# Optimization experiments

Measured on AMD Instinct MI355X. Metric: run time of the kernel, lower is better.

The kernel has to match this reference:

```python
import jax, jax.numpy as jnp
import numpy as np

N_NODES = 100000
N_EDGES = 800000
IN_FEAT = 128


def setup_inputs() -> dict:
    key = jax.random.key(0)
    k_feat, k_src, k_dst, k_w1, k_b1, k_w2 = jax.random.split(key, 6)
    feature = jax.random.normal(k_feat, (N_NODES, IN_FEAT), dtype=jnp.float32)
    src = jax.random.randint(k_src, (N_EDGES,), 0, N_NODES, dtype=jnp.int64)
    dst = jax.random.randint(k_dst, (N_EDGES,), 0, N_NODES, dtype=jnp.int64)
    # nn.Linear params: y = x @ W.T + b; Kaiming-uniform-ish init scale
    lim1 = 1.0 / np.sqrt(2 * IN_FEAT)
    W1 = jax.random.uniform(k_w1, (IN_FEAT, 2 * IN_FEAT), jnp.float32, -lim1, lim1)
    b1 = jax.random.uniform(k_b1, (IN_FEAT,), jnp.float32, -lim1, lim1)
    lim2 = 1.0 / np.sqrt(IN_FEAT)
    W2 = jax.random.uniform(k_w2, (1, IN_FEAT), jnp.float32, -lim2, lim2)
    b2 = jnp.zeros((1,), jnp.float32)
    return {"feature": feature, "src": src, "dst": dst,
            "W1": W1, "b1": b1, "W2": W2, "b2": b2}


def reference(feature, src, dst, W1, b1, W2, b2):
    # gather src/dst node feats and concat -> [E, 2*in_feat]
    h = jnp.concatenate([feature[src], feature[dst]], axis=1)
    # 2-layer MLP per edge: Linear -> ReLU -> Linear
    hid = jax.nn.relu(h @ W1.T + b1)            # [E, in_feat]
    score = hid @ W2.T + b2                      # [E, 1]
    return score
```

## Files before the change

### kernel.cpp

```cpp
#include <hip/hip_runtime.h>
#include <stdint.h>

typedef short short8 __attribute__((ext_vector_type(8)));
typedef float floatx4 __attribute__((ext_vector_type(4)));

#define NN 100000
#define NE 800000
#define KF 128
#define PC 256
#define BM 64
#define LDK 136

__device__ __forceinline__ unsigned short f2bf(float x) {
  union { float f; unsigned u; } c; c.f = x;
  unsigned u = c.u + 0x7FFFu + ((c.u >> 16) & 1u);
  return (unsigned short)(u >> 16);
}
__device__ __forceinline__ float bfl(unsigned u) {
  union { unsigned u; float f; } c; c.u = u << 16; return c.f;
}
__device__ __forceinline__ float bfh(unsigned u) {
  union { unsigned u; float f; } c; c.u = u & 0xFFFF0000u; return c.f;
}

extern "C" __global__ void __launch_bounds__(256)
wcat_prep_kernel(const float* __restrict__ W1, unsigned short* __restrict__ Wcatb)
{
  const int idx = blockIdx.x * 256 + threadIdx.x;
  const int j  = idx >> 4;
  const int k8 = (idx & 15) << 3;

  const int h  = j >> 7;
  const int jl = j & 127;
  const float* sp = W1 + (size_t)jl * 256 + h * 128 + k8;
  const float4 f0 = ((const float4*)sp)[0];
  const float4 f1 = ((const float4*)sp)[1];

  short8 v;
  v[0] = (short)f2bf(f0.x); v[1] = (short)f2bf(f0.y);
  v[2] = (short)f2bf(f0.z); v[3] = (short)f2bf(f0.w);
  v[4] = (short)f2bf(f1.x); v[5] = (short)f2bf(f1.y);
  v[6] = (short)f2bf(f1.z); v[7] = (short)f2bf(f1.w);

  const unsigned lin = (unsigned)jl * 256u + (unsigned)k8 * 2u;
  const unsigned swz = lin ^ ((unsigned)(jl & 7) << 4);
  *(short8*)((char*)Wcatb + h * 32768 + swz) = v;
}

extern "C" __global__ void __launch_bounds__(256)
node_proj_kernel(const float* __restrict__ feature,
                 const unsigned short* __restrict__ Wcatb,
                 const float* __restrict__ b1,
                 unsigned short* __restrict__ P)
{
  __shared__ unsigned short Wl[128 * 128];
  __shared__ unsigned short Al[BM * LDK];
  __shared__ float b1l[128];

  const int t = threadIdx.x;
  const int nodeBase = blockIdx.x * BM;

  #pragma unroll
  for (int it = 0; it < 8; ++it) {
    int c = t + it * 256;
    __builtin_amdgcn_global_load_lds(
        (const __attribute__((address_space(1))) void*)((const char*)Wcatb + c * 16),
        (__attribute__((address_space(3))) void*)((char*)Wl + c * 16),
        16, 0, 0);
  }

  #pragma unroll
  for (int it = 0; it < 4; ++it) {
    int c  = t + it * 256;
    int nl = c >> 4;
    int kc = (c & 15) << 3;
    int node = nodeBase + nl;
    float4 f0 = make_float4(0.f, 0.f, 0.f, 0.f);
    float4 f1 = make_float4(0.f, 0.f, 0.f, 0.f);
    if (node < NN) {
      const float* fp = feature + (size_t)node * KF + kc;
      f0 = ((const float4*)fp)[0];
      f1 = ((const float4*)fp)[1];
    }
    short8 v;
    v[0] = (short)f2bf(f0.x); v[1] = (short)f2bf(f0.y);
    v[2] = (short)f2bf(f0.z); v[3] = (short)f2bf(f0.w);
    v[4] = (short)f2bf(f1.x); v[5] = (short)f2bf(f1.y);
    v[6] = (short)f2bf(f1.z); v[7] = (short)f2bf(f1.w);
    *(short8*)&Al[nl * LDK + kc] = v;
  }
  if (t < 128) b1l[t] = b1[t];

  const int wave = t >> 6;
  const int lane = t & 63;
  const int m16  = lane & 15;
  const int quad = lane >> 4;

  short8 a0, a1, a2, a3;
  bool aLoaded = false;

  for (int half = 0; half < 2; ++half) {
    __syncthreads();

    if (!aLoaded) {
      const unsigned short* arow = &Al[(wave * 16 + m16) * LDK + quad * 8];
      a0 = *(const short8*)(arow + 0);
      a1 = *(const short8*)(arow + 32);
      a2 = *(const short8*)(arow + 64);
      a3 = *(const short8*)(arow + 96);
      aLoaded = true;
    }

    #pragma unroll
    for (int nt = 0; nt < 8; ++nt) {
      floatx4 acc = {0.f, 0.f, 0.f, 0.f};
      const int j = nt * 16 + m16;
      const unsigned base = (unsigned)j * 256u + (unsigned)quad * 16u;
      const unsigned msk  = (unsigned)(j & 7) << 4;
      const char* WlB = (const char*)Wl;
      acc = __builtin_amdgcn_mfma_f32_16x16x32_bf16(a0, *(const short8*)(WlB + ((base +   0u) ^ msk)), acc, 0, 0, 0);
      acc = __builtin_amdgcn_mfma_f32_16x16x32_bf16(a1, *(const short8*)(WlB + ((base +  64u) ^ msk)), acc, 0, 0, 0);
      acc = __builtin_amdgcn_mfma_f32_16x16x32_bf16(a2, *(const short8*)(WlB + ((base + 128u) ^ msk)), acc, 0, 0, 0);
      acc = __builtin_amdgcn_mfma_f32_16x16x32_bf16(a3, *(const short8*)(WlB + ((base + 192u) ^ msk)), acc, 0, 0, 0);

      const int n = half * 128 + j;
      const float bias = (half == 0) ? b1l[j] : 0.f;
      #pragma unroll
      for (int r = 0; r < 4; ++r) {
        int node = nodeBase + wave * 16 + quad * 4 + r;
        if (node < NN) P[(size_t)node * PC + n] = f2bf(acc[r] + bias);
      }
    }

    if (half == 0) {
      __syncthreads();
      #pragma unroll
      for (int it = 0; it < 8; ++it) {
        int c = t + it * 256;
        __builtin_amdgcn_global_load_lds(
            (const __attribute__((address_space(1))) void*)((const char*)Wcatb + 32768 + c * 16),
            (__attribute__((address_space(3))) void*)((char*)Wl + c * 16),
            16, 0, 0);
      }
    }
  }
}

__device__ __forceinline__ float dot8(const uint4 u1, const uint4 u2,
                                      const float4 wA, const float4 wB)
{
  float acc = 0.f, x;
  x = fmaxf(bfl(u1.x) + bfl(u2.x), 0.f); acc += x * wA.x;
  x = fmaxf(bfh(u1.x) + bfh(u2.x), 0.f); acc += x * wA.y;
  x = fmaxf(bfl(u1.y) + bfl(u2.y), 0.f); acc += x * wA.z;
  x = fmaxf(bfh(u1.y) + bfh(u2.y), 0.f); acc += x * wA.w;
  x = fmaxf(bfl(u1.z) + bfl(u2.z), 0.f); acc += x * wB.x;
  x = fmaxf(bfh(u1.z) + bfh(u2.z), 0.f); acc += x * wB.y;
  x = fmaxf(bfl(u1.w) + bfl(u2.w), 0.f); acc += x * wB.z;
  x = fmaxf(bfh(u1.w) + bfh(u2.w), 0.f); acc += x * wB.w;
  return acc;
}

extern "C" __global__ void __launch_bounds__(256)
edge_score_kernel(const unsigned short* __restrict__ P,
                  const int* __restrict__ src,
                  const int* __restrict__ dst,
                  const float* __restrict__ W2,
                  const float* __restrict__ b2,
                  float* __restrict__ out)
{
  const int t    = threadIdx.x;
  const int lane = t & 15;
  const int g    = t >> 4;
  const int e0   = blockIdx.x * 64 + g * 4;
  if (e0 >= NE) return;

  const int4 sv = *(const int4*)(src + e0);
  const int4 dv = *(const int4*)(dst + e0);

  const unsigned short* Ps = P + lane * 8;
  const unsigned short* Pd = P + 128 + lane * 8;

  const uint4 A0 = *(const uint4*)(Ps + (size_t)sv.x * PC);
  const uint4 B0 = *(const uint4*)(Pd + (size_t)dv.x * PC);
  const uint4 A1 = *(const uint4*)(Ps + (size_t)sv.y * PC);
  const uint4 B1 = *(const uint4*)(Pd + (size_t)dv.y * PC);
  const uint4 A2 = *(const uint4*)(Ps + (size_t)sv.z * PC);
  const uint4 B2 = *(const uint4*)(Pd + (size_t)dv.z * PC);
  const uint4 A3 = *(const uint4*)(Ps + (size_t)sv.w * PC);
  const uint4 B3 = *(const uint4*)(Pd + (size_t)dv.w * PC);

  const float4 wA = *(const float4*)(W2 + lane * 8);
  const float4 wB = *(const float4*)(W2 + lane * 8 + 4);

  float r0 = dot8(A0, B0, wA, wB);
  float r1 = dot8(A1, B1, wA, wB);
  float r2 = dot8(A2, B2, wA, wB);
  float r3 = dot8(A3, B3, wA, wB);

  r0 += __shfl_xor(r0, 8); r1 += __shfl_xor(r1, 8);
  r2 += __shfl_xor(r2, 8); r3 += __shfl_xor(r3, 8);
  r0 += __shfl_xor(r0, 4); r1 += __shfl_xor(r1, 4);
  r2 += __shfl_xor(r2, 4); r3 += __shfl_xor(r3, 4);
  r0 += __shfl_xor(r0, 2); r1 += __shfl_xor(r1, 2);
  r2 += __shfl_xor(r2, 2); r3 += __shfl_xor(r3, 2);
  r0 += __shfl_xor(r0, 1); r1 += __shfl_xor(r1, 1);
  r2 += __shfl_xor(r2, 1); r3 += __shfl_xor(r3, 1);

  if (lane == 0) {
    const float bb = b2[0];
    float4 o;
    o.x = r0 + bb; o.y = r1 + bb; o.z = r2 + bb; o.w = r3 + bb;
    *(float4*)(out + e0) = o;
  }
}

extern "C" void kernel_launch(void* const* d_in, const int* in_sizes, int n_in,
                              void* d_out, int out_size, void* d_ws, size_t ws_size,
                              hipStream_t stream)
{
  const float* feature = (const float*)d_in[0];
  const int*   src     = (const int*)d_in[1];
  const int*   dst     = (const int*)d_in[2];
  const float* W1      = (const float*)d_in[3];
  const float* b1      = (const float*)d_in[4];
  const float* W2      = (const float*)d_in[5];
  const float* b2      = (const float*)d_in[6];
  float* out = (float*)d_out;
  unsigned short* P = (unsigned short*)d_ws;
  unsigned short* Wcatb = (unsigned short*)d_out;

  dim3 gridW(16);
  wcat_prep_kernel<<<gridW, 256, 0, stream>>>(W1, Wcatb);

  dim3 grid1((NN + BM - 1) / BM);
  node_proj_kernel<<<grid1, 256, 0, stream>>>(feature, Wcatb, b1, P);

  dim3 grid2((NE + 63) / 64);
  edge_score_kernel<<<grid2, 256, 0, stream>>>(P, src, dst, W2, b2, out);
}
```

Measured before the change: 170.4 us.

## Quantize per-node projections to int8 with per-row scales for edge gather

The per-node projected hidden halves are now stored as int8 with a per-node, per-half absmax scale instead of bf16. This halves the bytes each edge gathers from the random-access projection table, and it also halves the projection write traffic. In exchange there is an extra scale gather per endpoint, a cross-lane max reduction in the projection kernel, and byte-wise stores with extra dequantization arithmetic. Accuracy loss from int8 rounding of pre-ReLU activations may exceed the tolerance.

Measured after the change: 144.5 us. -15.2%, faster.

```diff
diff --git a/kernel.cpp b/kernel.cpp
--- a/kernel.cpp
+++ b/kernel.cpp
@@ -16,11 +16,8 @@
   unsigned u = c.u + 0x7FFFu + ((c.u >> 16) & 1u);
   return (unsigned short)(u >> 16);
 }
-__device__ __forceinline__ float bfl(unsigned u) {
-  union { unsigned u; float f; } c; c.u = u << 16; return c.f;
-}
-__device__ __forceinline__ float bfh(unsigned u) {
-  union { unsigned u; float f; } c; c.u = u & 0xFFFF0000u; return c.f;
+__device__ __forceinline__ float sb8(unsigned u, int k) {
+  return (float)(signed char)((u >> (8 * k)) & 0xffu);
 }
 
 extern "C" __global__ void __launch_bounds__(256)
@@ -51,7 +48,8 @@
 node_proj_kernel(const float* __restrict__ feature,
                  const unsigned short* __restrict__ Wcatb,
                  const float* __restrict__ b1,
-                 unsigned short* __restrict__ P)
+                 signed char* __restrict__ P,
+                 float* __restrict__ Sc)
 {
   __shared__ unsigned short Wl[128 * 128];
   __shared__ unsigned short Al[BM * LDK];
@@ -111,6 +109,8 @@
       aLoaded = true;
     }
 
+    floatx4 arr[8];
+
     #pragma unroll
     for (int nt = 0; nt < 8; ++nt) {
       floatx4 acc = {0.f, 0.f, 0.f, 0.f};
@@ -122,14 +122,48 @@
       acc = __builtin_amdgcn_mfma_f32_16x16x32_bf16(a1, *(const short8*)(WlB + ((base +  64u) ^ msk)), acc, 0, 0, 0);
       acc = __builtin_amdgcn_mfma_f32_16x16x32_bf16(a2, *(const short8*)(WlB + ((base + 128u) ^ msk)), acc, 0, 0, 0);
       acc = __builtin_amdgcn_mfma_f32_16x16x32_bf16(a3, *(const short8*)(WlB + ((base + 192u) ^ msk)), acc, 0, 0, 0);
-
-      const int n = half * 128 + j;
-      const float bias = (half == 0) ? b1l[j] : 0.f;
-      #pragma unroll
-      for (int r = 0; r < 4; ++r) {
-        int node = nodeBase + wave * 16 + quad * 4 + r;
-        if (node < NN) P[(size_t)node * PC + n] = f2bf(acc[r] + bias);
+      if (half == 0) {
+        const float bias = b1l[j];
+        acc[0] += bias; acc[1] += bias; acc[2] += bias; acc[3] += bias;
       }
+      arr[nt] = acc;
+    }
+
+    float mx0 = 0.f, mx1 = 0.f, mx2 = 0.f, mx3 = 0.f;
+    #pragma unroll
+    for (int nt = 0; nt < 8; ++nt) {
+      mx0 = fmaxf(mx0, fabsf(arr[nt][0]));
+      mx1 = fmaxf(mx1, fabsf(arr[nt][1]));
+      mx2 = fmaxf(mx2, fabsf(arr[nt][2]));
+      mx3 = fmaxf(mx3, fabsf(arr[nt][3]));
+    }
+    #pragma unroll
+    for (int d_ = 1; d_ <= 8; d_ <<= 1) {
+      mx0 = fmaxf(mx0, __shfl_xor(mx0, d_));
+      mx1 = fmaxf(mx1, __shfl_xor(mx1, d_));
+      mx2 = fmaxf(mx2, __shfl_xor(mx2, d_));
+      mx3 = fmaxf(mx3, __shfl_xor(mx3, d_));
+    }
+    const float inv0 = 127.f / fmaxf(mx0, 1e-30f);
+    const float inv1 = 127.f / fmaxf(mx1, 1e-30f);
+    const float inv2 = 127.f / fmaxf(mx2, 1e-30f);
+    const float inv3 = 127.f / fmaxf(mx3, 1e-30f);
+
+    const int n0 = nodeBase + wave * 16 + quad * 4;
+    if (m16 == 0) {
+      if (n0 + 0 < NN) Sc[(size_t)(n0 + 0) * 2 + half] = mx0 * (1.f / 127.f);
+      if (n0 + 1 < NN) Sc[(size_t)(n0 + 1) * 2 + half] = mx1 * (1.f / 127.f);
+      if (n0 + 2 < NN) Sc[(size_t)(n0 + 2) * 2 + half] = mx2 * (1.f / 127.f);
+      if (n0 + 3 < NN) Sc[(size_t)(n0 + 3) * 2 + half] = mx3 * (1.f / 127.f);
+    }
+
+    #pragma unroll
+    for (int nt = 0; nt < 8; ++nt) {
+      const int off = half * 128 + nt * 16 + m16;
+      if (n0 + 0 < NN) P[(size_t)(n0 + 0) * PC + off] = (signed char)(int)rintf(arr[nt][0] * inv0);
+      if (n0 + 1 < NN) P[(size_t)(n0 + 1) * PC + off] = (signed char)(int)rintf(arr[nt][1] * inv1);
+      if (n0 + 2 < NN) P[(size_t)(n0 + 2) * PC + off] = (signed char)(int)rintf(arr[nt][2] * inv2);
+      if (n0 + 3 < NN) P[(size_t)(n0 + 3) * PC + off] = (signed char)(int)rintf(arr[nt][3] * inv3);
     }
 
     if (half == 0) {
@@ -146,23 +180,25 @@
   }
 }
 
-__device__ __forceinline__ float dot8(const uint4 u1, const uint4 u2,
-                                      const float4 wA, const float4 wB)
+__device__ __forceinline__ float dot8i8(const uint2 a, const uint2 b,
+                                        const float sa, const float sb,
+                                        const float* __restrict__ w)
 {
   float acc = 0.f, x;
-  x = fmaxf(bfl(u1.x) + bfl(u2.x), 0.f); acc += x * wA.x;
-  x = fmaxf(bfh(u1.x) + bfh(u2.x), 0.f); acc += x * wA.y;
-  x = fmaxf(bfl(u1.y) + bfl(u2.y), 0.f); acc += x * wA.z;
-  x = fmaxf(bfh(u1.y) + bfh(u2.y), 0.f); acc += x * wA.w;
-  x = fmaxf(bfl(u1.z) + bfl(u2.z), 0.f); acc += x * wB.x;
-  x = fmaxf(bfh(u1.z) + bfh(u2.z), 0.f); acc += x * wB.y;
-  x = fmaxf(bfl(u1.w) + bfl(u2.w), 0.f); acc += x * wB.z;
-  x = fmaxf(bfh(u1.w) + bfh(u2.w), 0.f); acc += x * wB.w;
+  x = fmaxf(fmaf(sb8(a.x, 0), sa, sb8(b.x, 0) * sb), 0.f); acc = fmaf(x, w[0], acc);
+  x = fmaxf(fmaf(sb8(a.x, 1), sa, sb8(b.x, 1) * sb), 0.f); acc = fmaf(x, w[1], acc);
+  x = fmaxf(fmaf(sb8(a.x, 2), sa, sb8(b.x, 2) * sb), 0.f); acc = fmaf(x, w[2], acc);
+  x = fmaxf(fmaf(sb8(a.x, 3), sa, sb8(b.x, 3) * sb), 0.f); acc = fmaf(x, w[3], acc);
+  x = fmaxf(fmaf(sb8(a.y, 0), sa, sb8(b.y, 0) * sb), 0.f); acc = fmaf(x, w[4], acc);
+  x = fmaxf(fmaf(sb8(a.y, 1), sa, sb8(b.y, 1) * sb), 0.f); acc = fmaf(x, w[5], acc);
+  x = fmaxf(fmaf(sb8(a.y, 2), sa, sb8(b.y, 2) * sb), 0.f); acc = fmaf(x, w[6], acc);
+  x = fmaxf(fmaf(sb8(a.y, 3), sa, sb8(b.y, 3) * sb), 0.f); acc = fmaf(x, w[7], acc);
   return acc;
 }
 
 extern "C" __global__ void __launch_bounds__(256)
-edge_score_kernel(const unsigned short* __restrict__ P,
+edge_score_kernel(const signed char* __restrict__ P,
+                  const float* __restrict__ Sc,
                   const int* __restrict__ src,
                   const int* __restrict__ dst,
                   const float* __restrict__ W2,
@@ -178,25 +214,39 @@
   const int4 sv = *(const int4*)(src + e0);
   const int4 dv = *(const int4*)(dst + e0);
 
-  const unsigned short* Ps = P + lane * 8;
-  const unsigned short* Pd = P + 128 + lane * 8;
-
-  const uint4 A0 = *(const uint4*)(Ps + (size_t)sv.x * PC);
-  const uint4 B0 = *(const uint4*)(Pd + (size_t)dv.x * PC);
-  const uint4 A1 = *(const uint4*)(Ps + (size_t)sv.y * PC);
-  const uint4 B1 = *(const uint4*)(Pd + (size_t)dv.y * PC);
-  const uint4 A2 = *(const uint4*)(Ps + (size_t)sv.z * PC);
-  const uint4 B2 = *(const uint4*)(Pd + (size_t)dv.z * PC);
-  const uint4 A3 = *(const uint4*)(Ps + (size_t)sv.w * PC);
-  const uint4 B3 = *(const uint4*)(Pd + (size_t)dv.w * PC);
-
-  const float4 wA = *(const float4*)(W2 + lane * 8);
-  const float4 wB = *(const float4*)(W2 + lane * 8 + 4);
-
-  float r0 = dot8(A0, B0, wA, wB);
-  float r1 = dot8(A1, B1, wA, wB);
-  float r2 = dot8(A2, B2, wA, wB);
-  float r3 = dot8(A3, B3, wA, wB);
+  const signed char* Ps = P + lane * 8;
+  const signed char* Pd = P + 128 + lane * 8;
+
+  const uint2 A0 = *(const uint2*)(Ps + (size_t)sv.x * PC);
+  const uint2 B0 = *(const uint2*)(Pd + (size_t)dv.x * PC);
+  const uint2 A1 = *(const uint2*)(Ps + (size_t)sv.y * PC);
+  const uint2 B1 = *(const uint2*)(Pd + (size_t)dv.y * PC);
+  const uint2 A2 = *(const uint2*)(Ps + (size_t)sv.z * PC);
+  const uint2 B2 = *(const uint2*)(Pd + (size_t)dv.z * PC);
+  const uint2 A3 = *(const uint2*)(Ps + (size_t)sv.w * PC);
+  const uint2 B3 = *(const uint2*)(Pd + (size_t)dv.w * PC);
+
+  const float sA0 = Sc[(size_t)sv.x * 2];
+  const float sB0 = Sc[(size_t)dv.x * 2 + 1];
+  const float sA1 = Sc[(size_t)sv.y * 2];
+  const float sB1 = Sc[(size_t)dv.y * 2 + 1];
+  const float sA2 = Sc[(size_t)sv.z * 2];
+  const float sB2 = Sc[(size_t)dv.z * 2 + 1];
+  const float sA3 = Sc[(size_t)sv.w * 2];
+  const float sB3 = Sc[(size_t)dv.w * 2 + 1];
+
+  float w[8];
+  {
+    const float4 wA = *(const float4*)(W2 + lane * 8);
+    const float4 wB = *(const float4*)(W2 + lane * 8 + 4);
+    w[0] = wA.x; w[1] = wA.y; w[2] = wA.z; w[3] = wA.w;
+    w[4] = wB.x; w[5] = wB.y; w[6] = wB.z; w[7] = wB.w;
+  }
+
+  float r0 = dot8i8(A0, B0, sA0, sB0, w);
+  float r1 = dot8i8(A1, B1, sA1, sB1, w);
+  float r2 = dot8i8(A2, B2, sA2, sB2, w);
+  float r3 = dot8i8(A3, B3, sA3, sB3, w);
 
   r0 += __shfl_xor(r0, 8); r1 += __shfl_xor(r1, 8);
   r2 += __shfl_xor(r2, 8); r3 += __shfl_xor(r3, 8);
@@ -227,15 +277,16 @@
   const float* W2      = (const float*)d_in[5];
   const float* b2      = (const float*)d_in[6];
   float* out = (float*)d_out;
-  unsigned short* P = (unsigned short*)d_ws;
+  signed char* P = (signed char*)d_ws;
+  float* Sc = (float*)((char*)d_ws + (size_t)NN * PC);
   unsigned short* Wcatb = (unsigned short*)d_out;
 
   dim3 gridW(16);
   wcat_prep_kernel<<<gridW, 256, 0, stream>>>(W1, Wcatb);
 
   dim3 grid1((NN + BM - 1) / BM);
-  node_proj_kernel<<<grid1, 256, 0, stream>>>(feature, Wcatb, b1, P);
+  node_proj_kernel<<<grid1, 256, 0, stream>>>(feature, Wcatb, b1, P, Sc);
 
   dim3 grid2((NE + 63) / 64);
-  edge_score_kernel<<<grid2, 256, 0, stream>>>(P, src, dst, W2, b2, out);
-}
+  edge_score_kernel<<<grid2, 256, 0, stream>>>(P, Sc, src, dst, W2, b2, out);
+}
```
